# Optimization experiments

Hardware: AMD Instinct MI355X
Metric: run time of the kernel (lower is better)

The kernel has to match this reference:

```python
import jax, jax.numpy as jnp
import numpy as np

B, N_HM, K_APP, S = 16, 32, 16, 256

def setup_inputs() -> dict:
    key = jax.random.key(0)
    k1, k2, k3 = jax.random.split(key, 3)
    # x: post-UNet appearance feature map [B, K, S, S]
    x = jax.random.normal(k1, (B, K_APP, S, S), dtype=jnp.float32)
    # raw_tps: raw heatmap logits [B, N, S, S]
    raw_tps = jax.random.normal(k2, (B, N_HM, S, S), dtype=jnp.float32)
    # fitted_cj: non-negative fitted heatmaps [B, N, S, S]
    fitted_cj = jax.random.uniform(k3, (B, N_HM, S, S), dtype=jnp.float32)
    return {"x": x, "raw_tps": raw_tps, "fitted_cj": fitted_cj}

def reference(x, raw_tps, fitted_cj):
    # torch F.softmax on a 2D [S,S] tensor with no dim defaults to dim=1 -> per-row softmax
    p = jax.nn.softmax(raw_tps, axis=-1)                      # [B, N, S, S]
    # attention pooling: app_vec[b,n,k] = sum_{h,w} x[b,k,h,w] * p[b,n,h,w]
    app_vec = jnp.einsum('bkhw,bnhw->bnk', x, p)              # [B, N, K]
    # weighted combine without materializing the [B,N,S,S,K] repeat
    num = jnp.einsum('bnhw,bnk->bhwk', fitted_cj, app_vec)    # [B, S, S, K]
    denom = 1.0 + jnp.sum(fitted_cj, axis=1)[..., None]       # [B, S, S, 1]
    app_enco = num / denom                                     # [B, S, S, K]
    # transpose(2,3) then transpose(1,2): [B,S,S,K] -> [B,K,S,S]
    return jnp.transpose(app_enco, (0, 3, 1, 2))
```

## Files before the change

### kernel.cpp

```cpp
#include <hip/hip_runtime.h>

#define S_DIM 256
#define N_HM 32
#define K_APP 16

template <bool ATOMIC>
__global__ __launch_bounds__(256, 4) void k1_softmax_pool(
    const float* __restrict__ x,
    const float* __restrict__ raw,
    float* __restrict__ outp)
{
    const int tid  = threadIdx.x;
    const int b    = blockIdx.x >> 8;
    const int h    = blockIdx.x & 255;
    const int wid  = tid >> 6;
    const int lane = tid & 63;
    const int kh   = wid >> 1;
    const int rh   = wid & 1;

    const float* xb = x + ((size_t)(b * K_APP + kh * 8) << 16) + (h << 8) + (lane << 2);
    float4 xv[8];
    #pragma unroll
    for (int j = 0; j < 8; ++j)
        xv[j] = *(const float4*)(xb + ((size_t)j << 16));

    const float* rb = raw + ((size_t)(b * N_HM + rh * 16) << 16) + (h << 8) + (lane << 2);
    float4 nxt = *(const float4*)rb;

    #pragma unroll
    for (int i = 0; i < 16; ++i) {
        float4 cur = nxt;
        if (i < 15) nxt = *(const float4*)(rb + ((size_t)(i + 1) << 16));

        float e0 = __expf(cur.x), e1 = __expf(cur.y);
        float e2 = __expf(cur.z), e3 = __expf(cur.w);
        float s = e0 + e1 + e2 + e3;
        #pragma unroll
        for (int off = 32; off > 0; off >>= 1) s += __shfl_xor(s, off);
        const float inv = 1.0f / s;

        float A[8];
        #pragma unroll
        for (int j = 0; j < 8; ++j)
            A[j] = e0 * xv[j].x + e1 * xv[j].y + e2 * xv[j].z + e3 * xv[j].w;

        #pragma unroll
        for (int j = 0; j < 4; ++j) {
            float send = (lane & 4) ? A[j] : A[j + 4];
            float keep = (lane & 4) ? A[j + 4] : A[j];
            A[j] = keep + __shfl_xor(send, 4);
        }
        #pragma unroll
        for (int j = 0; j < 2; ++j) {
            float send = (lane & 2) ? A[j] : A[j + 2];
            float keep = (lane & 2) ? A[j + 2] : A[j];
            A[j] = keep + __shfl_xor(send, 2);
        }
        {
            float send = (lane & 1) ? A[0] : A[1];
            float keep = (lane & 1) ? A[1] : A[0];
            A[0] = keep + __shfl_xor(send, 1);
        }
        float v = A[0];
        v += __shfl_xor(v, 8);
        v += __shfl_xor(v, 16);
        v += __shfl_xor(v, 32);
        v *= inv;

        const int n = rh * 16 + i;
        if (lane < 8) {
            if (ATOMIC)
                atomicAdd(outp + (b << 9) + (n << 4) + kh * 8 + lane, v);
            else
                outp[((size_t)blockIdx.x << 9) + (n << 4) + kh * 8 + lane] = v;
        }
    }
}

__global__ __launch_bounds__(256) void k1_reduce(
    const float* __restrict__ partial, float* __restrict__ av)
{
    __shared__ float s_lds[256];
    const int tid = threadIdx.x;
    const int o   = (blockIdx.x << 5) + (tid & 31);
    const int ch  = tid >> 5;
    const int b   = o >> 9;
    const int r   = o & 511;

    const float* p = partial + ((size_t)((b << 8) + (ch << 5)) << 9) + r;
    float s = 0.0f;
    #pragma unroll 8
    for (int j = 0; j < 32; ++j) s += p[(size_t)j << 9];

    s_lds[tid] = s;
    __syncthreads();
    if (tid < 32) {
        float t = s_lds[tid];
        #pragma unroll
        for (int c = 1; c < 8; ++c) t += s_lds[tid + (c << 5)];
        av[o] = t;
    }
}

__global__ __launch_bounds__(256, 4) void k2_combine(
    const float* __restrict__ fit,
    const float* __restrict__ av,
    float* __restrict__ out)
{
    const int tid = threadIdx.x;
    const int b   = blockIdx.x >> 6;
    const int hw4 = ((blockIdx.x & 63) << 8) + tid;

    const float*  avb = av + (b << 9);
    const float4* fb  = (const float4*)fit + ((size_t)(b * N_HM) << 14) + hw4;

    float4 num[16];
    #pragma unroll
    for (int k = 0; k < 16; ++k) num[k] = make_float4(0.f, 0.f, 0.f, 0.f);
    float dx = 1.f, dy = 1.f, dz = 1.f, dw = 1.f;

#define ACC(K, AS)                                                         \
    num[K].x += f.x * (AS); num[K].y += f.y * (AS);                        \
    num[K].z += f.z * (AS); num[K].w += f.w * (AS);

    #pragma unroll 8
    for (int n = 0; n < N_HM; ++n) {
        float4 f = fb[(size_t)n << 14];
        dx += f.x; dy += f.y; dz += f.z; dw += f.w;
        const float4* ar = (const float4*)(avb + (n << 4));
        float4 a0 = ar[0], a1 = ar[1], a2 = ar[2], a3 = ar[3];
        ACC(0,  a0.x) ACC(1,  a0.y) ACC(2,  a0.z) ACC(3,  a0.w)
        ACC(4,  a1.x) ACC(5,  a1.y) ACC(6,  a1.z) ACC(7,  a1.w)
        ACC(8,  a2.x) ACC(9,  a2.y) ACC(10, a2.z) ACC(11, a2.w)
        ACC(12, a3.x) ACC(13, a3.y) ACC(14, a3.z) ACC(15, a3.w)
    }
#undef ACC

    const float ix = 1.f / dx, iy = 1.f / dy, iz = 1.f / dz, iw = 1.f / dw;
    float4* ob = (float4*)out + ((size_t)(b * K_APP) << 14) + hw4;
    #pragma unroll
    for (int k = 0; k < 16; ++k)
        ob[(size_t)k << 14] = make_float4(num[k].x * ix, num[k].y * iy,
                                          num[k].z * iz, num[k].w * iw);
}

extern "C" void kernel_launch(void* const* d_in, const int* in_sizes, int n_in,
                              void* d_out, int out_size, void* d_ws, size_t ws_size,
                              hipStream_t stream)
{
    const float* x   = (const float*)d_in[0];
    const float* raw = (const float*)d_in[1];
    const float* fit = (const float*)d_in[2];
    float* out = (float*)d_out;

    float* av      = (float*)d_ws;
    float* partial = (float*)d_ws + 8192;
    const size_t need = (size_t)(8192 + 4096 * 512) * sizeof(float);

    if (ws_size >= need) {
        k1_softmax_pool<false><<<4096, 256, 0, stream>>>(x, raw, partial);
        k1_reduce<<<256, 256, 0, stream>>>(partial, av);
    } else {
        hipMemsetAsync(av, 0, 8192 * sizeof(float), stream);
        k1_softmax_pool<true><<<4096, 256, 0, stream>>>(x, raw, av);
    }
    k2_combine<<<1024, 256, 0, stream>>>(fit, av, out);
}
```

Before: 349.4 us.

## Have each wave handle all 16 channels over 8 heatmaps in softmax-pool

The softmax-pool kernel now has each wave hold all 16 x channels in registers and handle 8 heatmap rows, instead of splitting channels and heatmaps across waves. This means each raw_tps row is read and exponentiated once per block rather than twice, halving the redundant exp/softmax-sum work. The cost is more registers (16 float4 pinned with empty asm), one extra butterfly shuffle stage, and possibly lower occupancy.

```diff
diff --git a/kernel.cpp b/kernel.cpp
--- a/kernel.cpp
+++ b/kernel.cpp
@@ -15,22 +15,25 @@
     const int h    = blockIdx.x & 255;
     const int wid  = tid >> 6;
     const int lane = tid & 63;
-    const int kh   = wid >> 1;
-    const int rh   = wid & 1;
 
-    const float* xb = x + ((size_t)(b * K_APP + kh * 8) << 16) + (h << 8) + (lane << 2);
-    float4 xv[8];
+    const float* xb = x + ((size_t)(b * K_APP) << 16) + (h << 8) + (lane << 2);
+    float4 xv[K_APP];
     #pragma unroll
-    for (int j = 0; j < 8; ++j)
-        xv[j] = *(const float4*)(xb + ((size_t)j << 16));
+    for (int k = 0; k < K_APP; ++k)
+        xv[k] = *(const float4*)(xb + ((size_t)k << 16));
+    #pragma unroll
+    for (int k = 0; k < K_APP; ++k)
+        asm volatile("" : "+v"(xv[k].x), "+v"(xv[k].y),
+                          "+v"(xv[k].z), "+v"(xv[k].w));
 
-    const float* rb = raw + ((size_t)(b * N_HM + rh * 16) << 16) + (h << 8) + (lane << 2);
-    float4 nxt = *(const float4*)rb;
+    const float* rb = raw + ((size_t)(b * N_HM) << 16) + (h << 8) + (lane << 2);
+    float4 nxt = *(const float4*)(rb + ((size_t)(wid * 8) << 16));
 
     #pragma unroll
-    for (int i = 0; i < 16; ++i) {
+    for (int i = 0; i < 8; ++i) {
+        const int n = wid * 8 + i;
         float4 cur = nxt;
-        if (i < 15) nxt = *(const float4*)(rb + ((size_t)(i + 1) << 16));
+        if (i < 7) nxt = *(const float4*)(rb + ((size_t)(n + 1) << 16));
 
         float e0 = __expf(cur.x), e1 = __expf(cur.y);
         float e2 = __expf(cur.z), e3 = __expf(cur.w);
@@ -39,11 +42,17 @@
         for (int off = 32; off > 0; off >>= 1) s += __shfl_xor(s, off);
         const float inv = 1.0f / s;
 
-        float A[8];
+        float A[16];
         #pragma unroll
-        for (int j = 0; j < 8; ++j)
-            A[j] = e0 * xv[j].x + e1 * xv[j].y + e2 * xv[j].z + e3 * xv[j].w;
+        for (int k = 0; k < K_APP; ++k)
+            A[k] = e0 * xv[k].x + e1 * xv[k].y + e2 * xv[k].z + e3 * xv[k].w;
 
+        #pragma unroll
+        for (int j = 0; j < 8; ++j) {
+            float send = (lane & 8) ? A[j] : A[j + 8];
+            float keep = (lane & 8) ? A[j + 8] : A[j];
+            A[j] = keep + __shfl_xor(send, 8);
+        }
         #pragma unroll
         for (int j = 0; j < 4; ++j) {
             float send = (lane & 4) ? A[j] : A[j + 4];
@@ -62,17 +71,15 @@
             A[0] = keep + __shfl_xor(send, 1);
         }
         float v = A[0];
-        v += __shfl_xor(v, 8);
         v += __shfl_xor(v, 16);
         v += __shfl_xor(v, 32);
         v *= inv;
 
-        const int n = rh * 16 + i;
-        if (lane < 8) {
+        if (lane < 16) {
             if (ATOMIC)
-                atomicAdd(outp + (b << 9) + (n << 4) + kh * 8 + lane, v);
+                atomicAdd(outp + (b << 9) + (n << 4) + lane, v);
             else
-                outp[((size_t)blockIdx.x << 9) + (n << 4) + kh * 8 + lane] = v;
+                outp[((size_t)blockIdx.x << 9) + (n << 4) + lane] = v;
         }
     }
 }
```

Result: no change. 348.9 us (-0.1%).

## Fuse softmax-pool, reduce and combine into one cooperative kernel with grid syncs

Applied to the files above, without the earlier changes.

Replaces the three separate launches with a single cooperative kernel of 1024 blocks that runs the softmax-pooling stage (four rows per block, two heatmaps per loop iteration), a grid-wide sync, the partial reduction, another grid sync, and then the combine stage. The aim is to remove launch gaps and inter-kernel drain. In exchange, the pooling phase has only 1024 blocks instead of 4096, and the grid syncs cost time. Each block now also processes four rows serially with unroll 1, which may reduce latency hiding. If the cooperative launch fails, the code falls back to the old three-kernel path.

```diff
diff --git a/kernel.cpp b/kernel.cpp
--- a/kernel.cpp
+++ b/kernel.cpp
@@ -1,13 +1,174 @@
 #include <hip/hip_runtime.h>
+#include <hip/hip_cooperative_groups.h>
+
+namespace cg = cooperative_groups;
 
 #define S_DIM 256
 #define N_HM 32
 #define K_APP 16
 
+__global__ __launch_bounds__(256, 4) void fused_all(
+    const float* __restrict__ x,
+    const float* __restrict__ raw,
+    const float* __restrict__ fit,
+    float* __restrict__ out,
+    float* __restrict__ partial,
+    float* __restrict__ av)
+{
+    cg::grid_group grid = cg::this_grid();
+    __shared__ float s_lds[256];
+
+    const int tid  = threadIdx.x;
+    const int bid  = blockIdx.x;
+    const int wid  = tid >> 6;
+    const int lane = tid & 63;
+    const int kh   = wid >> 1;
+    const int rh   = wid & 1;
+
+    #pragma unroll 1
+    for (int j = 0; j < 4; ++j) {
+        const int u = (bid << 2) + j;
+        const int b = u >> 8;
+        const int h = u & 255;
+
+        const float* xb = x + ((size_t)(b * K_APP + kh * 8) << 16) + (h << 8) + (lane << 2);
+        float4 xv[8];
+        #pragma unroll
+        for (int q = 0; q < 8; ++q)
+            xv[q] = *(const float4*)(xb + ((size_t)q << 16));
+
+        const float* rb = raw + ((size_t)(b * N_HM + rh * 16) << 16) + (h << 8) + (lane << 2);
+        float4 p0 = *(const float4*)rb;
+        float4 p1 = *(const float4*)(rb + ((size_t)1 << 16));
+
+        #pragma unroll
+        for (int i = 0; i < 16; i += 2) {
+            float4 c0 = p0, c1 = p1;
+            if (i < 14) {
+                p0 = *(const float4*)(rb + ((size_t)(i + 2) << 16));
+                p1 = *(const float4*)(rb + ((size_t)(i + 3) << 16));
+            }
+
+            float e00 = __expf(c0.x), e01 = __expf(c0.y), e02 = __expf(c0.z), e03 = __expf(c0.w);
+            float e10 = __expf(c1.x), e11 = __expf(c1.y), e12 = __expf(c1.z), e13 = __expf(c1.w);
+            float s0 = e00 + e01 + e02 + e03;
+            float s1 = e10 + e11 + e12 + e13;
+            #pragma unroll
+            for (int off = 32; off > 0; off >>= 1) {
+                s0 += __shfl_xor(s0, off);
+                s1 += __shfl_xor(s1, off);
+            }
+            const float inv0 = 1.0f / s0, inv1 = 1.0f / s1;
+
+            float A0[8], A1[8];
+            #pragma unroll
+            for (int q = 0; q < 8; ++q) {
+                A0[q] = e00 * xv[q].x + e01 * xv[q].y + e02 * xv[q].z + e03 * xv[q].w;
+                A1[q] = e10 * xv[q].x + e11 * xv[q].y + e12 * xv[q].z + e13 * xv[q].w;
+            }
+
+            #pragma unroll
+            for (int q = 0; q < 4; ++q) {
+                float sa = (lane & 4) ? A0[q] : A0[q + 4];
+                float ka = (lane & 4) ? A0[q + 4] : A0[q];
+                A0[q] = ka + __shfl_xor(sa, 4);
+                float sb = (lane & 4) ? A1[q] : A1[q + 4];
+                float kb = (lane & 4) ? A1[q + 4] : A1[q];
+                A1[q] = kb + __shfl_xor(sb, 4);
+            }
+            #pragma unroll
+            for (int q = 0; q < 2; ++q) {
+                float sa = (lane & 2) ? A0[q] : A0[q + 2];
+                float ka = (lane & 2) ? A0[q + 2] : A0[q];
+                A0[q] = ka + __shfl_xor(sa, 2);
+                float sb = (lane & 2) ? A1[q] : A1[q + 2];
+                float kb = (lane & 2) ? A1[q + 2] : A1[q];
+                A1[q] = kb + __shfl_xor(sb, 2);
+            }
+            {
+                float sa = (lane & 1) ? A0[0] : A0[1];
+                float ka = (lane & 1) ? A0[1] : A0[0];
+                A0[0] = ka + __shfl_xor(sa, 1);
+                float sb = (lane & 1) ? A1[0] : A1[1];
+                float kb = (lane & 1) ? A1[1] : A1[0];
+                A1[0] = kb + __shfl_xor(sb, 1);
+            }
+            float v0 = A0[0], v1 = A1[0];
+            v0 += __shfl_xor(v0, 8);  v1 += __shfl_xor(v1, 8);
+            v0 += __shfl_xor(v0, 16); v1 += __shfl_xor(v1, 16);
+            v0 += __shfl_xor(v0, 32); v1 += __shfl_xor(v1, 32);
+            v0 *= inv0; v1 *= inv1;
+
+            if (lane < 8) {
+                float* dst = partial + ((size_t)u << 9)
+                           + ((rh * 16 + i) << 4) + kh * 8 + lane;
+                dst[0]  = v0;
+                dst[16] = v1;
+            }
+        }
+    }
+    grid.sync();
+
+    {
+        const int o  = (bid << 3) + (tid & 7);
+        const int ch = tid >> 3;
+        const int b  = o >> 9;
+        const int r  = o & 511;
+        const float* p = partial + ((size_t)((b << 8) + (ch << 3)) << 9) + r;
+        float s = 0.0f;
+        #pragma unroll
+        for (int q = 0; q < 8; ++q) s += p[(size_t)q << 9];
+        s_lds[tid] = s;
+        __syncthreads();
+        if (tid < 8) {
+            float t = s_lds[tid];
+            #pragma unroll
+            for (int c = 1; c < 32; ++c) t += s_lds[tid + (c << 3)];
+            av[o] = t;
+        }
+    }
+    grid.sync();
+
+    {
+        const int b   = bid >> 6;
+        const int hw4 = ((bid & 63) << 8) + tid;
+        const float*  avb = av + (b << 9);
+        const float4* fb  = (const float4*)fit + ((size_t)(b * N_HM) << 14) + hw4;
+
+        float4 num[16];
+        #pragma unroll
+        for (int k = 0; k < 16; ++k) num[k] = make_float4(0.f, 0.f, 0.f, 0.f);
+        float dx = 1.f, dy = 1.f, dz = 1.f, dw = 1.f;
+
+#define ACC(K, AS)                                                         \
+        num[K].x += f.x * (AS); num[K].y += f.y * (AS);                    \
+        num[K].z += f.z * (AS); num[K].w += f.w * (AS);
+
+        #pragma unroll 8
+        for (int n = 0; n < N_HM; ++n) {
+            float4 f = fb[(size_t)n << 14];
+            dx += f.x; dy += f.y; dz += f.z; dw += f.w;
+            const float4* ar = (const float4*)(avb + (n << 4));
+            float4 a0 = ar[0], a1 = ar[1], a2 = ar[2], a3 = ar[3];
+            ACC(0,  a0.x) ACC(1,  a0.y) ACC(2,  a0.z) ACC(3,  a0.w)
+            ACC(4,  a1.x) ACC(5,  a1.y) ACC(6,  a1.z) ACC(7,  a1.w)
+            ACC(8,  a2.x) ACC(9,  a2.y) ACC(10, a2.z) ACC(11, a2.w)
+            ACC(12, a3.x) ACC(13, a3.y) ACC(14, a3.z) ACC(15, a3.w)
+        }
+#undef ACC
+
+        const float ix = 1.f / dx, iy = 1.f / dy, iz = 1.f / dz, iw = 1.f / dw;
+        float4* ob = (float4*)out + ((size_t)(b * K_APP) << 14) + hw4;
+        #pragma unroll
+        for (int k = 0; k < 16; ++k)
+            ob[(size_t)k << 14] = make_float4(num[k].x * ix, num[k].y * iy,
+                                              num[k].z * iz, num[k].w * iw);
+    }
+}
+
 template <bool ATOMIC>
 __global__ __launch_bounds__(256, 4) void k1_softmax_pool(
-    const float* __restrict__ x,
-    const float* __restrict__ raw,
+    const float* __restrict__ x, const float* __restrict__ raw,
     float* __restrict__ outp)
 {
     const int tid  = threadIdx.x;
@@ -21,8 +182,8 @@
     const float* xb = x + ((size_t)(b * K_APP + kh * 8) << 16) + (h << 8) + (lane << 2);
     float4 xv[8];
     #pragma unroll
-    for (int j = 0; j < 8; ++j)
-        xv[j] = *(const float4*)(xb + ((size_t)j << 16));
+    for (int q = 0; q < 8; ++q)
+        xv[q] = *(const float4*)(xb + ((size_t)q << 16));
 
     const float* rb = raw + ((size_t)(b * N_HM + rh * 16) << 16) + (h << 8) + (lane << 2);
     float4 nxt = *(const float4*)rb;
@@ -31,42 +192,38 @@
     for (int i = 0; i < 16; ++i) {
         float4 cur = nxt;
         if (i < 15) nxt = *(const float4*)(rb + ((size_t)(i + 1) << 16));
-
         float e0 = __expf(cur.x), e1 = __expf(cur.y);
         float e2 = __expf(cur.z), e3 = __expf(cur.w);
         float s = e0 + e1 + e2 + e3;
         #pragma unroll
         for (int off = 32; off > 0; off >>= 1) s += __shfl_xor(s, off);
         const float inv = 1.0f / s;
-
         float A[8];
         #pragma unroll
-        for (int j = 0; j < 8; ++j)
-            A[j] = e0 * xv[j].x + e1 * xv[j].y + e2 * xv[j].z + e3 * xv[j].w;
-
-        #pragma unroll
-        for (int j = 0; j < 4; ++j) {
-            float send = (lane & 4) ? A[j] : A[j + 4];
-            float keep = (lane & 4) ? A[j + 4] : A[j];
-            A[j] = keep + __shfl_xor(send, 4);
-        }
-        #pragma unroll
-        for (int j = 0; j < 2; ++j) {
-            float send = (lane & 2) ? A[j] : A[j + 2];
-            float keep = (lane & 2) ? A[j + 2] : A[j];
-            A[j] = keep + __shfl_xor(send, 2);
+        for (int q = 0; q < 8; ++q)
+            A[q] = e0 * xv[q].x + e1 * xv[q].y + e2 * xv[q].z + e3 * xv[q].w;
+        #pragma unroll
+        for (int q = 0; q < 4; ++q) {
+            float sa = (lane & 4) ? A[q] : A[q + 4];
+            float ka = (lane & 4) ? A[q + 4] : A[q];
+            A[q] = ka + __shfl_xor(sa, 4);
+        }
+        #pragma unroll
+        for (int q = 0; q < 2; ++q) {
+            float sa = (lane & 2) ? A[q] : A[q + 2];
+            float ka = (lane & 2) ? A[q + 2] : A[q];
+            A[q] = ka + __shfl_xor(sa, 2);
         }
         {
-            float send = (lane & 1) ? A[0] : A[1];
-            float keep = (lane & 1) ? A[1] : A[0];
-            A[0] = keep + __shfl_xor(send, 1);
+            float sa = (lane & 1) ? A[0] : A[1];
+            float ka = (lane & 1) ? A[1] : A[0];
+            A[0] = ka + __shfl_xor(sa, 1);
         }
         float v = A[0];
         v += __shfl_xor(v, 8);
         v += __shfl_xor(v, 16);
         v += __shfl_xor(v, 32);
         v *= inv;
-
         const int n = rh * 16 + i;
         if (lane < 8) {
             if (ATOMIC)
@@ -86,12 +243,10 @@
     const int ch  = tid >> 5;
     const int b   = o >> 9;
     const int r   = o & 511;
-
     const float* p = partial + ((size_t)((b << 8) + (ch << 5)) << 9) + r;
     float s = 0.0f;
     #pragma unroll 8
     for (int j = 0; j < 32; ++j) s += p[(size_t)j << 9];
-
     s_lds[tid] = s;
     __syncthreads();
     if (tid < 32) {
@@ -103,26 +258,21 @@
 }
 
 __global__ __launch_bounds__(256, 4) void k2_combine(
-    const float* __restrict__ fit,
-    const float* __restrict__ av,
+    const float* __restrict__ fit, const float* __restrict__ av,
     float* __restrict__ out)
 {
     const int tid = threadIdx.x;
     const int b   = blockIdx.x >> 6;
     const int hw4 = ((blockIdx.x & 63) << 8) + tid;
-
     const float*  avb = av + (b << 9);
     const float4* fb  = (const float4*)fit + ((size_t)(b * N_HM) << 14) + hw4;
-
     float4 num[16];
     #pragma unroll
     for (int k = 0; k < 16; ++k) num[k] = make_float4(0.f, 0.f, 0.f, 0.f);
     float dx = 1.f, dy = 1.f, dz = 1.f, dw = 1.f;
-
 #define ACC(K, AS)                                                         \
     num[K].x += f.x * (AS); num[K].y += f.y * (AS);                        \
     num[K].z += f.z * (AS); num[K].w += f.w * (AS);
-
     #pragma unroll 8
     for (int n = 0; n < N_HM; ++n) {
         float4 f = fb[(size_t)n << 14];
@@ -135,7 +285,6 @@
         ACC(12, a3.x) ACC(13, a3.y) ACC(14, a3.z) ACC(15, a3.w)
     }
 #undef ACC
-
     const float ix = 1.f / dx, iy = 1.f / dy, iz = 1.f / dz, iw = 1.f / dw;
     float4* ob = (float4*)out + ((size_t)(b * K_APP) << 14) + hw4;
     #pragma unroll
@@ -157,12 +306,27 @@
     float* partial = (float*)d_ws + 8192;
     const size_t need = (size_t)(8192 + 4096 * 512) * sizeof(float);
 
+    bool fused_ok = false;
     if (ws_size >= need) {
-        k1_softmax_pool<false><<<4096, 256, 0, stream>>>(x, raw, partial);
-        k1_reduce<<<256, 256, 0, stream>>>(partial, av);
-    } else {
-        hipMemsetAsync(av, 0, 8192 * sizeof(float), stream);
-        k1_softmax_pool<true><<<4096, 256, 0, stream>>>(x, raw, av);
-    }
-    k2_combine<<<1024, 256, 0, stream>>>(fit, av, out);
-}
+        void* args[] = { (void*)&x, (void*)&raw, (void*)&fit,
+                         (void*)&out, (void*)&partial, (void*)&av };
+        hipError_t err = hipLaunchCooperativeKernel(
+            (const void*)fused_all, dim3(1024), dim3(256), args, 0, stream);
+        if (err == hipSuccess) {
+            fused_ok = true;
+        } else {
+            (void)hipGetLastError();
+        }
+    }
+
+    if (!fused_ok) {
+        if (ws_size >= need) {
+            k1_softmax_pool<false><<<4096, 256, 0, stream>>>(x, raw, partial);
+            k1_reduce<<<256, 256, 0, stream>>>(partial, av);
+        } else {
+            hipMemsetAsync(av, 0, 8192 * sizeof(float), stream);
+            k1_softmax_pool<true><<<4096, 256, 0, stream>>>(x, raw, av);
+        }
+        k2_combine<<<1024, 256, 0, stream>>>(fit, av, out);
+    }
+}
```

Result: slower. 598.1 us (+71.2%).

## Compute softmax-weighted pooling with bf16 MFMA using hi/lo split of x

Applied to the files above, without the earlier changes.

Replaces the per-row shuffle-reduction dot products in the pooling kernel with MFMA 16x16x32 bf16 matrix multiplies. Exponentials are staged to LDS as bf16, x is split into bf16 high and low parts for extra precision, and the row sums come from an MFMA against a ones vector. Each block now handles two rows, so the grid is halved and occupancy hints change. This aims to cut VALU and cross-lane shuffle cost, at the price of bf16 rounding of the exponentials and added LDS traffic.

```diff
diff --git a/kernel.cpp b/kernel.cpp
--- a/kernel.cpp
+++ b/kernel.cpp
@@ -3,76 +3,93 @@
 #define S_DIM 256
 #define N_HM 32
 #define K_APP 16
+#define LDW 264
+
+typedef __bf16 b16x8 __attribute__((ext_vector_type(8)));
+typedef float  f32x4 __attribute__((ext_vector_type(4)));
+
+__device__ __forceinline__ unsigned short f2bf(float f) {
+    unsigned u = __builtin_bit_cast(unsigned, f);
+    unsigned r = u + 0x7FFFu + ((u >> 16) & 1u);
+    return (unsigned short)(r >> 16);
+}
+__device__ __forceinline__ float bf2f(unsigned short s) {
+    return __builtin_bit_cast(float, (unsigned)s << 16);
+}
 
 template <bool ATOMIC>
-__global__ __launch_bounds__(256, 4) void k1_softmax_pool(
+__global__ __launch_bounds__(256, 2) void k1_softmax_pool(
     const float* __restrict__ x,
     const float* __restrict__ raw,
     float* __restrict__ outp)
 {
+    __shared__ unsigned short eA[4][16][LDW];
+    __shared__ unsigned short xH[2][16][LDW];
+    __shared__ unsigned short xL[2][16][LDW];
+
     const int tid  = threadIdx.x;
-    const int b    = blockIdx.x >> 8;
-    const int h    = blockIdx.x & 255;
-    const int wid  = tid >> 6;
+    const int wv   = tid >> 6;
     const int lane = tid & 63;
-    const int kh   = wid >> 1;
-    const int rh   = wid & 1;
+    const int hsel = wv & 1;
+    const int rg   = wv >> 1;
+    const int u    = (blockIdx.x << 1) + hsel;
+    const int b    = u >> 8;
+    const int h    = u & 255;
 
-    const float* xb = x + ((size_t)(b * K_APP + kh * 8) << 16) + (h << 8) + (lane << 2);
-    float4 xv[8];
+    {
+        const float* xb = x + ((size_t)(b * K_APP + rg * 8) << 16) + (h << 8) + (lane << 2);
+        #pragma unroll
+        for (int q = 0; q < 8; ++q) {
+            float4 v = *(const float4*)(xb + ((size_t)q << 16));
+            const int k = rg * 8 + q;
+            unsigned short h0 = f2bf(v.x), h1 = f2bf(v.y), h2 = f2bf(v.z), h3 = f2bf(v.w);
+            unsigned short l0 = f2bf(v.x - bf2f(h0)), l1 = f2bf(v.y - bf2f(h1));
+            unsigned short l2 = f2bf(v.z - bf2f(h2)), l3 = f2bf(v.w - bf2f(h3));
+            *(ushort4*)&xH[hsel][k][lane << 2] = make_ushort4(h0, h1, h2, h3);
+            *(ushort4*)&xL[hsel][k][lane << 2] = make_ushort4(l0, l1, l2, l3);
+        }
+    }
+
+    {
+        const float* rb = raw + ((size_t)(b * N_HM + rg * 16) << 16) + (h << 8) + (lane << 2);
+        #pragma unroll
+        for (int i = 0; i < 16; ++i) {
+            float4 v = *(const float4*)(rb + ((size_t)i << 16));
+            *(ushort4*)&eA[wv][i][lane << 2] =
+                make_ushort4(f2bf(__expf(v.x)), f2bf(__expf(v.y)),
+                             f2bf(__expf(v.z)), f2bf(__expf(v.w)));
+        }
+    }
+    __syncthreads();
+
+    f32x4 acc  = {0.f, 0.f, 0.f, 0.f};
+    f32x4 sacc = {0.f, 0.f, 0.f, 0.f};
+    b16x8 ones;
     #pragma unroll
-    for (int j = 0; j < 8; ++j)
-        xv[j] = *(const float4*)(xb + ((size_t)j << 16));
+    for (int j = 0; j < 8; ++j) ones[j] = (__bf16)1.0f;
 
-    const float* rb = raw + ((size_t)(b * N_HM + rh * 16) << 16) + (h << 8) + (lane << 2);
-    float4 nxt = *(const float4*)rb;
+    const int frow = lane & 15;
+    const int fcol = (lane >> 4) << 3;
 
     #pragma unroll
-    for (int i = 0; i < 16; ++i) {
-        float4 cur = nxt;
-        if (i < 15) nxt = *(const float4*)(rb + ((size_t)(i + 1) << 16));
+    for (int st = 0; st < 8; ++st) {
+        b16x8 a  = *(const b16x8*)&eA[wv][frow][fcol + (st << 5)];
+        b16x8 bh = *(const b16x8*)&xH[hsel][frow][fcol + (st << 5)];
+        b16x8 bl = *(const b16x8*)&xL[hsel][frow][fcol + (st << 5)];
+        acc  = __builtin_amdgcn_mfma_f32_16x16x32_bf16(a, bh, acc, 0, 0, 0);
+        acc  = __builtin_amdgcn_mfma_f32_16x16x32_bf16(a, bl, acc, 0, 0, 0);
+        sacc = __builtin_amdgcn_mfma_f32_16x16x32_bf16(a, ones, sacc, 0, 0, 0);
+    }
 
-        float e0 = __expf(cur.x), e1 = __expf(cur.y);
-        float e2 = __expf(cur.z), e3 = __expf(cur.w);
-        float s = e0 + e1 + e2 + e3;
-        #pragma unroll
-        for (int off = 32; off > 0; off >>= 1) s += __shfl_xor(s, off);
-        const float inv = 1.0f / s;
-
-        float A[8];
-        #pragma unroll
-        for (int j = 0; j < 8; ++j)
-            A[j] = e0 * xv[j].x + e1 * xv[j].y + e2 * xv[j].z + e3 * xv[j].w;
-
-        #pragma unroll
-        for (int j = 0; j < 4; ++j) {
-            float send = (lane & 4) ? A[j] : A[j + 4];
-            float keep = (lane & 4) ? A[j + 4] : A[j];
-            A[j] = keep + __shfl_xor(send, 4);
-        }
-        #pragma unroll
-        for (int j = 0; j < 2; ++j) {
-            float send = (lane & 2) ? A[j] : A[j + 2];
-            float keep = (lane & 2) ? A[j + 2] : A[j];
-            A[j] = keep + __shfl_xor(send, 2);
-        }
-        {
-            float send = (lane & 1) ? A[0] : A[1];
-            float keep = (lane & 1) ? A[1] : A[0];
-            A[0] = keep + __shfl_xor(send, 1);
-        }
-        float v = A[0];
-        v += __shfl_xor(v, 8);
-        v += __shfl_xor(v, 16);
-        v += __shfl_xor(v, 32);
-        v *= inv;
-
-        const int n = rh * 16 + i;
-        if (lane < 8) {
-            if (ATOMIC)
-                atomicAdd(outp + (b << 9) + (n << 4) + kh * 8 + lane, v);
-            else
-                outp[((size_t)blockIdx.x << 9) + (n << 4) + kh * 8 + lane] = v;
+    #pragma unroll
+    for (int r = 0; r < 4; ++r) {
+        const int rowl = ((lane >> 4) << 2) + r;
+        const int n    = (rg << 4) + rowl;
+        const float v  = acc[r] * __builtin_amdgcn_rcpf(sacc[r]);
+        if (ATOMIC) {
+            atomicAdd(outp + (b << 9) + (n << 4) + (lane & 15), v);
+        } else {
+            outp[((size_t)u << 9) + (n << 4) + (lane & 15)] = v;
         }
     }
 }
@@ -158,11 +175,11 @@
     const size_t need = (size_t)(8192 + 4096 * 512) * sizeof(float);
 
     if (ws_size >= need) {
-        k1_softmax_pool<false><<<4096, 256, 0, stream>>>(x, raw, partial);
+        k1_softmax_pool<false><<<2048, 256, 0, stream>>>(x, raw, partial);
         k1_reduce<<<256, 256, 0, stream>>>(partial, av);
     } else {
         hipMemsetAsync(av, 0, 8192 * sizeof(float), stream);
-        k1_softmax_pool<true><<<4096, 256, 0, stream>>>(x, raw, av);
+        k1_softmax_pool<true><<<2048, 256, 0, stream>>>(x, raw, av);
     }
     k2_combine<<<1024, 256, 0, stream>>>(fit, av, out);
 }
```

New measurement: 340.5 us. 1.03x faster.
